# Kernel optimization log

Measured on AMD Instinct MI355X. Metric: run time of the kernel, lower is better.

Reference implementation:

```python
import math
import jax, jax.numpy as jnp
import numpy as np

FIRE_THRESH = 0.85
_C = math.sqrt(2.0 / math.pi)

def _normalize(v, axis=-1, eps=1e-12):
    # matches torch F.normalize: v / max(||v||, eps)
    n = jnp.linalg.norm(v, axis=axis, keepdims=True)
    return v / jnp.maximum(n, eps)

def setup_inputs() -> dict:
    key = jax.random.key(0)
    k1, k2, k3 = jax.random.split(key, 3)
    B, T, D, N = 8, 4096, 1024, 512
    x = jax.random.normal(k1, (B, T, D), dtype=jnp.float32)
    buf = jax.random.normal(k2, (N, D), dtype=jnp.float32)
    depl = jax.random.uniform(k3, (N,), dtype=jnp.float32)
    mask = jnp.ones((N,), dtype=bool)
    ptr = 3  # static ring-buffer write position
    log_k = jnp.asarray(math.log(2.0), dtype=jnp.float32)
    logit_depl_rate = jnp.asarray(0.0, dtype=jnp.float32)
    logit_floor = jnp.asarray(math.log(0.1 / 0.9), dtype=jnp.float32)
    return {"x": x, "buf": buf, "depl": depl, "mask": mask, "ptr": ptr,
            "log_k": log_k, "logit_depl_rate": logit_depl_rate, "logit_floor": logit_floor}

def reference(x, buf, depl, mask, ptr, log_k, logit_depl_rate, logit_floor):
    # steady-state (_ready=True) forward of GELU244
    k_gate = jnp.clip(jnp.exp(log_k), 0.1, 8.0)
    depl_rate = 0.1 + 0.8 * jax.nn.sigmoid(logit_depl_rate)
    floor_val = 0.5 * jax.nn.sigmoid(logit_floor)
    # tanh-approx GELU
    y = 0.5 * x * (1.0 + jnp.tanh(_C * (x + 0.044715 * x ** 3)))  # [B,T,D]
    D = x.shape[-1]
    m_curr = jax.lax.stop_gradient(jnp.mean(y.reshape(-1, D), axis=0))  # [D]
    m_n = _normalize(m_curr, axis=0)  # unit vector [D]
    buf_n = _normalize(buf, axis=-1)  # [N,D]
    sims = jnp.where(mask, buf_n @ m_n, -1.0)  # [N]
    idx = jnp.argmax(sims)
    max_sim = sims[idx]
    depl_level = depl[idx]
    # .item() in torch => no grad through k_gate / depl_level here
    raw_gate = jnp.exp(-jax.lax.stop_gradient(k_gate) * (1.0 - jax.lax.stop_gradient(depl_level)))
    gate = floor_val + (1.0 - floor_val) * raw_gate
    output = y * gate
    # no_grad state update: deplete fired slot, write m_n at ring pointer
    factor = jnp.where(max_sim > FIRE_THRESH, jax.lax.stop_gradient(depl_rate), 1.0)
    new_depl = depl.at[idx].multiply(factor)
    new_buf = buf.at[ptr].set(m_n)
    new_depl = new_depl.at[ptr].set(1.0)
    new_mask = mask.at[ptr].set(True)
    return output, new_buf, new_depl, new_mask
```

## Files before the change

kernel.cpp:

```cpp
#include <hip/hip_runtime.h>
#include <math.h>

#define D_DIM    1024
#define D4       256
#define A_BLOCKS 1024
#define N_SLOTS  512

#define GK1 0.07135481627f
#define GK2 1.59576912161f

__device__ __forceinline__ float gelu_tanh(float x) {
    float t = x * __builtin_fmaf(GK1, x * x, GK2);
    float e = __expf(-t);
    return x * __builtin_amdgcn_rcpf(1.0f + e);
}

__global__ __launch_bounds__(256) void colsum_partial(
        const float* __restrict__ x, float* __restrict__ partial,
        int rows, int rows_per_block) {
    int t = threadIdx.x;
    int b = blockIdx.x;
    const float4* x4 = (const float4*)x;
    float4 acc = make_float4(0.f, 0.f, 0.f, 0.f);
    int r0 = b * rows_per_block;
    int r1 = min(r0 + rows_per_block, rows);
    #pragma unroll 4
    for (int r = r0; r < r1; ++r) {
        float4 v = x4[(size_t)r * D4 + t];
        acc.x += gelu_tanh(v.x);
        acc.y += gelu_tanh(v.y);
        acc.z += gelu_tanh(v.z);
        acc.w += gelu_tanh(v.w);
    }
    ((float4*)partial)[(size_t)b * D4 + t] = acc;
}

__global__ __launch_bounds__(256) void reduce_cols(
        const float* __restrict__ partial, float* __restrict__ s_out) {
    __shared__ float red[8][32];
    int t  = threadIdx.x, b = blockIdx.x;
    int cl = t & 31, sl = t >> 5;
    int c  = b * 32 + cl;
    float s = 0.f;
    int p0 = sl * (A_BLOCKS / 8);
    #pragma unroll 4
    for (int p = p0; p < p0 + A_BLOCKS / 8; ++p)
        s += partial[(size_t)p * D_DIM + c];
    red[sl][cl] = s;
    __syncthreads();
    if (t < 32) {
        float tot = 0.f;
        #pragma unroll
        for (int i = 0; i < 8; ++i) tot += red[i][t];
        s_out[b * 32 + t] = tot;
    }
}

__global__ __launch_bounds__(256) void sims_norm(
        const float* __restrict__ buf, const float* __restrict__ s_vec,
        float* __restrict__ snorm_out, float* __restrict__ dotraw,
        float* __restrict__ out_buf, const int* __restrict__ ptr_p,
        float eps_s) {
    int n = blockIdx.x, t = threadIdx.x;
    int wid = t >> 6, lane = t & 63;
    if (n == N_SLOTS) {
        float4 w = ((const float4*)s_vec)[t];
        float sq = w.x*w.x + w.y*w.y + w.z*w.z + w.w*w.w;
        #pragma unroll
        for (int off = 32; off > 0; off >>= 1) sq += __shfl_down(sq, off, 64);
        __shared__ float rs[4];
        if (lane == 0) rs[wid] = sq;
        __syncthreads();
        if (t == 0)
            snorm_out[0] = fmaxf(sqrtf(rs[0] + rs[1] + rs[2] + rs[3]), eps_s);
        return;
    }
    float4 v = ((const float4*)(buf + (size_t)n * D_DIM))[t];
    float4 w = ((const float4*)s_vec)[t];
    float dot = v.x*w.x + v.y*w.y + v.z*w.z + v.w*w.w;
    float sq  = v.x*v.x + v.y*v.y + v.z*v.z + v.w*v.w;
    #pragma unroll
    for (int off = 32; off > 0; off >>= 1) {
        dot += __shfl_down(dot, off, 64);
        sq  += __shfl_down(sq,  off, 64);
    }
    __shared__ float rd[4], rs2[4];
    if (lane == 0) { rd[wid] = dot; rs2[wid] = sq; }
    __syncthreads();
    if (t == 0) {
        float dd = rd[0] + rd[1] + rd[2] + rd[3];
        float ss = rs2[0] + rs2[1] + rs2[2] + rs2[3];
        dotraw[n] = dd / fmaxf(sqrtf(ss), 1e-12f);
    }
    if (n != ptr_p[0])
        ((float4*)(out_buf + (size_t)n * D_DIM))[t] = v;
}

__global__ __launch_bounds__(512) void gate_state(
        const float* __restrict__ dotraw, const float* __restrict__ snorm_p,
        const float* __restrict__ s_vec, const float* __restrict__ depl,
        const float* __restrict__ log_k, const float* __restrict__ logit_depl_rate,
        const float* __restrict__ logit_floor, const int* __restrict__ ptr_p,
        float* __restrict__ gate_out, float* __restrict__ out_depl,
        float* __restrict__ out_mask, float* __restrict__ out_buf) {
    __shared__ float sval[512];
    __shared__ int   sidx[512];
    int t = threadIdx.x;
    sval[t] = dotraw[t];
    sidx[t] = t;
    __syncthreads();
    for (int s = 256; s > 0; s >>= 1) {
        if (t < s) {
            float a = sval[t], b = sval[t + s];
            int ia = sidx[t], ib = sidx[t + s];
            if (b > a || (b == a && ib < ia)) { sval[t] = b; sidx[t] = ib; }
        }
        __syncthreads();
    }
    __shared__ float sfac;
    __shared__ int   sIdx;
    float snorm = snorm_p[0];
    if (t == 0) {
        int idx = sidx[0];
        float max_sim = sval[0] / snorm;
        float k_gate    = fminf(fmaxf(__expf(log_k[0]), 0.1f), 8.0f);
        float depl_rate = 0.1f + 0.8f / (1.0f + __expf(-logit_depl_rate[0]));
        float floor_val = 0.5f / (1.0f + __expf(-logit_floor[0]));
        float raw_gate  = __expf(-k_gate * (1.0f - depl[idx]));
        gate_out[0] = floor_val + (1.0f - floor_val) * raw_gate;
        sfac = (max_sim > 0.85f) ? depl_rate : 1.0f;
        sIdx = idx;
    }
    __syncthreads();
    int ptr = ptr_p[0];
    float nd = depl[t] * (t == sIdx ? sfac : 1.0f);
    if (t == ptr) nd = 1.0f;
    out_depl[t] = nd;
    out_mask[t] = 1.0f;
    out_buf[(size_t)ptr * D_DIM + t]       = s_vec[t]       / snorm;
    out_buf[(size_t)ptr * D_DIM + t + 512] = s_vec[t + 512] / snorm;
}

__global__ __launch_bounds__(256) void gelu_gate_out(
        const float* __restrict__ x, const float* __restrict__ gate_p,
        float* __restrict__ out, int n4) {
    float gate = gate_p[0];
    int stride = gridDim.x * blockDim.x;
    const float4* x4 = (const float4*)x;
    float4* o4 = (float4*)out;
    #pragma unroll 4
    for (int i = blockIdx.x * blockDim.x + threadIdx.x; i < n4; i += stride) {
        float4 v = x4[i];
        float4 r;
        r.x = gelu_tanh(v.x) * gate;
        r.y = gelu_tanh(v.y) * gate;
        r.z = gelu_tanh(v.z) * gate;
        r.w = gelu_tanh(v.w) * gate;
        o4[i] = r;
    }
}

extern "C" void kernel_launch(void* const* d_in, const int* in_sizes, int n_in,
                              void* d_out, int out_size, void* d_ws, size_t ws_size,
                              hipStream_t stream) {
    const float* x     = (const float*)d_in[0];
    const float* buf   = (const float*)d_in[1];
    const float* depl  = (const float*)d_in[2];
    const int*   ptr_p = (const int*)d_in[4];
    const float* log_k = (const float*)d_in[5];
    const float* ldr   = (const float*)d_in[6];
    const float* lf    = (const float*)d_in[7];

    int xN   = in_sizes[0];
    int bufN = in_sizes[1];
    int rows = xN / D_DIM;

    float* out      = (float*)d_out;
    float* out_buf  = out + xN;
    float* out_depl = out_buf + bufN;
    float* out_mask = out_depl + N_SLOTS;

    float* ws      = (float*)d_ws;
    float* s_vec   = ws;
    float* snorm   = ws + 1024;
    float* gate    = ws + 1025;
    float* dotraw  = ws + 1040;
    float* partial = ws + 2048;

    int rpb = (rows + A_BLOCKS - 1) / A_BLOCKS;
    float eps_s = 1e-12f * (float)rows;

    hipLaunchKernelGGL(colsum_partial, dim3(A_BLOCKS), dim3(256), 0, stream,
                       x, partial, rows, rpb);
    hipLaunchKernelGGL(reduce_cols, dim3(32), dim3(256), 0, stream,
                       partial, s_vec);
    hipLaunchKernelGGL(sims_norm, dim3(N_SLOTS + 1), dim3(256), 0, stream,
                       buf, s_vec, snorm, dotraw, out_buf, ptr_p, eps_s);
    hipLaunchKernelGGL(gate_state, dim3(1), dim3(512), 0, stream,
                       dotraw, snorm, s_vec, depl, log_k, ldr, lf, ptr_p,
                       gate, out_depl, out_mask, out_buf);
    hipLaunchKernelGGL(gelu_gate_out, dim3(2048), dim3(256), 0, stream,
                       x, gate, out, xN / 4);
}
```

Before: 86.91 us.

## Fuse gate computation into output kernel and move buffer copy into colsum pass

Removes the single-block gate_state kernel: every block of the output streaming kernel now redundantly recomputes the argmax over the 512 sims and the gate scalar, and block 0 also writes the depl, mask and new buffer row. The buffer copy moves from the sims kernel into the colsum kernel, and the colsum loop drops its bounds clamp and uses a larger unroll. This cuts two kernel launches and their serialization bubbles, at the cost of a redundant small reduction in each of the 2048 blocks. The colsum change assumes rows divides evenly by the block count.

```diff
diff --git a/kernel.cpp b/kernel.cpp
--- a/kernel.cpp
+++ b/kernel.cpp
@@ -5,6 +5,7 @@
 #define D4       256
 #define A_BLOCKS 1024
 #define N_SLOTS  512
+#define OUT_GRID 2048
 
 #define GK1 0.07135481627f
 #define GK2 1.59576912161f
@@ -16,16 +17,19 @@
 }
 
 __global__ __launch_bounds__(256) void colsum_partial(
-        const float* __restrict__ x, float* __restrict__ partial,
-        int rows, int rows_per_block) {
+        const float* __restrict__ x, const float* __restrict__ buf,
+        float* __restrict__ partial, float* __restrict__ out_buf,
+        const int* __restrict__ ptr_p, int rows, int rows_per_block) {
     int t = threadIdx.x;
     int b = blockIdx.x;
+    if (b < N_SLOTS && b != ptr_p[0])
+        ((float4*)(out_buf + (size_t)b * D_DIM))[t] =
+            ((const float4*)(buf + (size_t)b * D_DIM))[t];
     const float4* x4 = (const float4*)x;
     float4 acc = make_float4(0.f, 0.f, 0.f, 0.f);
     int r0 = b * rows_per_block;
-    int r1 = min(r0 + rows_per_block, rows);
-    #pragma unroll 4
-    for (int r = r0; r < r1; ++r) {
+    #pragma unroll 8
+    for (int r = r0; r < r0 + rows_per_block; ++r) {
         float4 v = x4[(size_t)r * D4 + t];
         acc.x += gelu_tanh(v.x);
         acc.y += gelu_tanh(v.y);
@@ -56,25 +60,11 @@
     }
 }
 
-__global__ __launch_bounds__(256) void sims_norm(
+__global__ __launch_bounds__(256) void sims_dot(
         const float* __restrict__ buf, const float* __restrict__ s_vec,
-        float* __restrict__ snorm_out, float* __restrict__ dotraw,
-        float* __restrict__ out_buf, const int* __restrict__ ptr_p,
-        float eps_s) {
+        float* __restrict__ dotraw) {
     int n = blockIdx.x, t = threadIdx.x;
     int wid = t >> 6, lane = t & 63;
-    if (n == N_SLOTS) {
-        float4 w = ((const float4*)s_vec)[t];
-        float sq = w.x*w.x + w.y*w.y + w.z*w.z + w.w*w.w;
-        #pragma unroll
-        for (int off = 32; off > 0; off >>= 1) sq += __shfl_down(sq, off, 64);
-        __shared__ float rs[4];
-        if (lane == 0) rs[wid] = sq;
-        __syncthreads();
-        if (t == 0)
-            snorm_out[0] = fmaxf(sqrtf(rs[0] + rs[1] + rs[2] + rs[3]), eps_s);
-        return;
-    }
     float4 v = ((const float4*)(buf + (size_t)n * D_DIM))[t];
     float4 w = ((const float4*)s_vec)[t];
     float dot = v.x*w.x + v.y*w.y + v.z*w.z + v.w*w.w;
@@ -84,72 +74,89 @@
         dot += __shfl_down(dot, off, 64);
         sq  += __shfl_down(sq,  off, 64);
     }
-    __shared__ float rd[4], rs2[4];
-    if (lane == 0) { rd[wid] = dot; rs2[wid] = sq; }
+    __shared__ float rd[4], rs[4];
+    if (lane == 0) { rd[wid] = dot; rs[wid] = sq; }
     __syncthreads();
-    if (t == 0) {
-        float dd = rd[0] + rd[1] + rd[2] + rd[3];
-        float ss = rs2[0] + rs2[1] + rs2[2] + rs2[3];
-        dotraw[n] = dd / fmaxf(sqrtf(ss), 1e-12f);
-    }
-    if (n != ptr_p[0])
-        ((float4*)(out_buf + (size_t)n * D_DIM))[t] = v;
-}
-
-__global__ __launch_bounds__(512) void gate_state(
-        const float* __restrict__ dotraw, const float* __restrict__ snorm_p,
+    if (t == 0)
+        dotraw[n] = (rd[0] + rd[1] + rd[2] + rd[3]) /
+                    fmaxf(sqrtf(rs[0] + rs[1] + rs[2] + rs[3]), 1e-12f);
+}
+
+__global__ __launch_bounds__(256) void gate_stream_out(
+        const float* __restrict__ x, const float* __restrict__ dotraw,
         const float* __restrict__ s_vec, const float* __restrict__ depl,
         const float* __restrict__ log_k, const float* __restrict__ logit_depl_rate,
         const float* __restrict__ logit_floor, const int* __restrict__ ptr_p,
-        float* __restrict__ gate_out, float* __restrict__ out_depl,
-        float* __restrict__ out_mask, float* __restrict__ out_buf) {
-    __shared__ float sval[512];
-    __shared__ int   sidx[512];
-    int t = threadIdx.x;
-    sval[t] = dotraw[t];
-    sidx[t] = t;
-    __syncthreads();
-    for (int s = 256; s > 0; s >>= 1) {
-        if (t < s) {
-            float a = sval[t], b = sval[t + s];
-            int ia = sidx[t], ib = sidx[t + s];
-            if (b > a || (b == a && ib < ia)) { sval[t] = b; sidx[t] = ib; }
+        float* __restrict__ out, float* __restrict__ out_buf,
+        float* __restrict__ out_depl, float* __restrict__ out_mask,
+        int n4, float eps_s) {
+    __shared__ float sval[256];
+    __shared__ int   sidx[256];
+    __shared__ float sgate;
+    int t = threadIdx.x, b = blockIdx.x;
+
+    {
+        float a  = dotraw[t];
+        float b2 = dotraw[t + 256];
+        float v; int id;
+        if (b2 > a) { v = b2; id = t + 256; } else { v = a; id = t; }
+        sval[t] = v; sidx[t] = id;
+        __syncthreads();
+        for (int s = 128; s > 0; s >>= 1) {
+            if (t < s) {
+                float av = sval[t], bv = sval[t + s];
+                int   ai = sidx[t], bi = sidx[t + s];
+                if (bv > av || (bv == av && bi < ai)) { sval[t] = bv; sidx[t] = bi; }
+            }
+            __syncthreads();
         }
-        __syncthreads();
-    }
-    __shared__ float sfac;
-    __shared__ int   sIdx;
-    float snorm = snorm_p[0];
-    if (t == 0) {
+        if (t == 0) {
+            int idx = sidx[0];
+            float k_gate    = fminf(fmaxf(__expf(log_k[0]), 0.1f), 8.0f);
+            float floor_val = 0.5f / (1.0f + __expf(-logit_floor[0]));
+            float raw_gate  = __expf(-k_gate * (1.0f - depl[idx]));
+            sgate = floor_val + (1.0f - floor_val) * raw_gate;
+        }
+        __syncthreads();
+    }
+
+    if (b == 0) {
+        float4 w0 = ((const float4*)s_vec)[t];
+        float sq = w0.x*w0.x + w0.y*w0.y + w0.z*w0.z + w0.w*w0.w;
+        #pragma unroll
+        for (int off = 32; off > 0; off >>= 1) sq += __shfl_down(sq, off, 64);
+        __shared__ float rs2[4];
+        __shared__ float ssnorm;
+        int wid = t >> 6, lane = t & 63;
+        if (lane == 0) rs2[wid] = sq;
+        __syncthreads();
+        if (t == 0)
+            ssnorm = fmaxf(sqrtf(rs2[0] + rs2[1] + rs2[2] + rs2[3]), eps_s);
+        __syncthreads();
+        float snorm = ssnorm;
         int idx = sidx[0];
-        float max_sim = sval[0] / snorm;
-        float k_gate    = fminf(fmaxf(__expf(log_k[0]), 0.1f), 8.0f);
+        int ptr = ptr_p[0];
+        float max_sim   = sval[0] / snorm;
         float depl_rate = 0.1f + 0.8f / (1.0f + __expf(-logit_depl_rate[0]));
-        float floor_val = 0.5f / (1.0f + __expf(-logit_floor[0]));
-        float raw_gate  = __expf(-k_gate * (1.0f - depl[idx]));
-        gate_out[0] = floor_val + (1.0f - floor_val) * raw_gate;
-        sfac = (max_sim > 0.85f) ? depl_rate : 1.0f;
-        sIdx = idx;
-    }
-    __syncthreads();
-    int ptr = ptr_p[0];
-    float nd = depl[t] * (t == sIdx ? sfac : 1.0f);
-    if (t == ptr) nd = 1.0f;
-    out_depl[t] = nd;
-    out_mask[t] = 1.0f;
-    out_buf[(size_t)ptr * D_DIM + t]       = s_vec[t]       / snorm;
-    out_buf[(size_t)ptr * D_DIM + t + 512] = s_vec[t + 512] / snorm;
-}
-
-__global__ __launch_bounds__(256) void gelu_gate_out(
-        const float* __restrict__ x, const float* __restrict__ gate_p,
-        float* __restrict__ out, int n4) {
-    float gate = gate_p[0];
-    int stride = gridDim.x * blockDim.x;
+        float fac = (max_sim > 0.85f) ? depl_rate : 1.0f;
+        #pragma unroll
+        for (int j = t; j < N_SLOTS; j += 256) {
+            float nd = depl[j] * (j == idx ? fac : 1.0f);
+            if (j == ptr) nd = 1.0f;
+            out_depl[j] = nd;
+            out_mask[j] = 1.0f;
+        }
+        float inv = 1.0f / snorm;
+        float4 sv = ((const float4*)s_vec)[t];
+        float4 mn = make_float4(sv.x*inv, sv.y*inv, sv.z*inv, sv.w*inv);
+        ((float4*)(out_buf + (size_t)ptr * D_DIM))[t] = mn;
+    }
+
+    float gate = sgate;
     const float4* x4 = (const float4*)x;
     float4* o4 = (float4*)out;
     #pragma unroll 4
-    for (int i = blockIdx.x * blockDim.x + threadIdx.x; i < n4; i += stride) {
+    for (int i = b * 256 + t; i < n4; i += OUT_GRID * 256) {
         float4 v = x4[i];
         float4 r;
         r.x = gelu_tanh(v.x) * gate;
@@ -182,23 +189,19 @@
 
     float* ws      = (float*)d_ws;
     float* s_vec   = ws;
-    float* snorm   = ws + 1024;
-    float* gate    = ws + 1025;
     float* dotraw  = ws + 1040;
     float* partial = ws + 2048;
 
-    int rpb = (rows + A_BLOCKS - 1) / A_BLOCKS;
+    int rpb = rows / A_BLOCKS;
     float eps_s = 1e-12f * (float)rows;
 
     hipLaunchKernelGGL(colsum_partial, dim3(A_BLOCKS), dim3(256), 0, stream,
-                       x, partial, rows, rpb);
+                       x, buf, partial, out_buf, ptr_p, rows, rpb);
     hipLaunchKernelGGL(reduce_cols, dim3(32), dim3(256), 0, stream,
                        partial, s_vec);
-    hipLaunchKernelGGL(sims_norm, dim3(N_SLOTS + 1), dim3(256), 0, stream,
-                       buf, s_vec, snorm, dotraw, out_buf, ptr_p, eps_s);
-    hipLaunchKernelGGL(gate_state, dim3(1), dim3(512), 0, stream,
-                       dotraw, snorm, s_vec, depl, log_k, ldr, lf, ptr_p,
-                       gate, out_depl, out_mask, out_buf);
-    hipLaunchKernelGGL(gelu_gate_out, dim3(2048), dim3(256), 0, stream,
-                       x, gate, out, xN / 4);
-}
+    hipLaunchKernelGGL(sims_dot, dim3(N_SLOTS), dim3(256), 0, stream,
+                       buf, s_vec, dotraw);
+    hipLaunchKernelGGL(gate_stream_out, dim3(OUT_GRID), dim3(256), 0, stream,
+                       x, dotraw, s_vec, depl, log_k, ldr, lf, ptr_p,
+                       out, out_buf, out_depl, out_mask, xN / 4, eps_s);
+}
```

Measured after the change: 85.61 us. No clear change (-1.5%).
